# Kernel optimization log

Hardware: AMD Instinct MI355X
Metric: run time of the kernel (lower is better)

## Reference

```python
import jax, jax.numpy as jnp
import numpy as np

N = 50000
E = 800000
IN_CH = 128
HID = 64
HEADS = 4
EPS = 1e-5
NEG_SLOPE = 0.2


def _gat_conv(x, src, dst, W, a_src, a_dst, b, heads, out_ch, concat):
    n = x.shape[0]
    h = (x @ W).reshape(n, heads, out_ch)                      # [N,H,C]
    alpha_src = jnp.sum(h * a_src, axis=-1)                    # [N,H]
    alpha_dst = jnp.sum(h * a_dst, axis=-1)                    # [N,H]
    e = jax.nn.leaky_relu(alpha_src[src] + alpha_dst[dst], NEG_SLOPE)  # [E',H]
    # segment softmax over incoming edges of each destination node
    m = jax.ops.segment_max(e, dst, num_segments=n)            # [N,H]
    e = jnp.exp(e - m[dst])
    denom = jax.ops.segment_sum(e, dst, num_segments=n)        # [N,H]
    alpha = e / denom[dst]                                     # [E',H]
    msg = h[src] * alpha[:, :, None]                           # [E',H,C]
    out = jax.ops.segment_sum(msg, dst, num_segments=n)        # [N,H,C]
    if concat:
        out = out.reshape(n, heads * out_ch)
    else:
        out = out.mean(axis=1)
    return out + b


def _bn_eval(x, gamma, beta, mean, var):
    return (x - mean) * (gamma / jnp.sqrt(var + EPS)) + beta


def setup_inputs() -> dict:
    key = jax.random.key(0)
    ks = jax.random.split(key, 24)
    s = 0.1
    x = jax.random.normal(ks[0], (N, IN_CH), dtype=jnp.float32)
    edge_index = jax.random.randint(ks[1], (2, E), 0, N, dtype=jnp.int32)
    d0, d1 = IN_CH, HID * HEADS
    inp = {
        'x': x, 'edge_index': edge_index,
        # layer 0: in_ch -> hidden, heads=4, concat
        'W0': jax.random.normal(ks[2], (d0, HEADS * HID), jnp.float32) * s,
        'as0': jax.random.normal(ks[3], (HEADS, HID), jnp.float32) * s,
        'ad0': jax.random.normal(ks[4], (HEADS, HID), jnp.float32) * s,
        'b0': jax.random.normal(ks[5], (HEADS * HID,), jnp.float32) * s,
        # layer 1: hidden*heads -> hidden, heads=4, concat
        'W1': jax.random.normal(ks[6], (d1, HEADS * HID), jnp.float32) * s,
        'as1': jax.random.normal(ks[7], (HEADS, HID), jnp.float32) * s,
        'ad1': jax.random.normal(ks[8], (HEADS, HID), jnp.float32) * s,
        'b1': jax.random.normal(ks[9], (HEADS * HID,), jnp.float32) * s,
        # layer 2: hidden*heads -> 1, heads=1, no concat
        'W2': jax.random.normal(ks[10], (d1, 1), jnp.float32) * s,
        'as2': jax.random.normal(ks[11], (1, 1), jnp.float32) * s,
        'ad2': jax.random.normal(ks[12], (1, 1), jnp.float32) * s,
        'b2': jax.random.normal(ks[13], (1,), jnp.float32) * s,
        # batchnorm (eval) params for the two hidden layers
        'g0': jnp.ones((d1,), jnp.float32),
        'be0': jnp.zeros((d1,), jnp.float32),
        'm0': jax.random.normal(ks[14], (d1,), jnp.float32) * s,
        'v0': jnp.ones((d1,), jnp.float32),
        'g1': jnp.ones((d1,), jnp.float32),
        'be1': jnp.zeros((d1,), jnp.float32),
        'm1': jax.random.normal(ks[15], (d1,), jnp.float32) * s,
        'v1': jnp.ones((d1,), jnp.float32),
    }
    return inp


def reference(x, edge_index, W0, as0, ad0, b0, W1, as1, ad1, b1,
              W2, as2, ad2, b2, g0, be0, m0, v0, g1, be1, m1, v1):
    n = x.shape[0]
    loops = jnp.arange(n, dtype=edge_index.dtype)
    src = jnp.concatenate([edge_index[0], loops])  # add self-loops (PyG default)
    dst = jnp.concatenate([edge_index[1], loops])

    # layer 0 (no residual: shapes differ)
    h = _gat_conv(x, src, dst, W0, as0, ad0, b0, HEADS, HID, True)
    h = jax.nn.elu(_bn_eval(h, g0, be0, m0, v0))

    # layer 1 (residual: shapes match)
    res = h
    h = _gat_conv(h, src, dst, W1, as1, ad1, b1, HEADS, HID, True)
    h = jax.nn.elu(_bn_eval(h, g1, be1, m1, v1)) + res

    # output layer: heads=1, concat=False -> [N,1]
    out = _gat_conv(h, src, dst, W2, as2, ad2, b2, 1, 1, False)
    return out.squeeze(-1)
```

## Files before the change

kernel.cpp:

```cpp
#include <hip/hip_runtime.h>
#include <math.h>

#define NEG_SLOPE 0.2f
#define BN_EPS 1e-5f

typedef __attribute__((ext_vector_type(8))) short bf16x8;
typedef __attribute__((ext_vector_type(4))) float f32x4;

static __device__ __forceinline__ unsigned short f2bf(float f){
    unsigned u = __float_as_uint(f);
    u += 0x7FFFu + ((u >> 16) & 1u);
    return (unsigned short)(u >> 16);
}
static __device__ __forceinline__ float bf2f(unsigned short v){
    return __uint_as_float((unsigned)v << 16);
}

static __device__ __forceinline__ void gload_lds16(const void* g, void* l){
    __builtin_amdgcn_global_load_lds(
        (const __attribute__((address_space(1))) void*)g,
        (__attribute__((address_space(3))) void*)l, 16, 0, 0);
}

static __device__ __forceinline__ void repack_one(const float* __restrict__ W,
    unsigned short* __restrict__ whi, unsigned short* __restrict__ wlo, int o)
{
    const int j = o & 7, ln = (o >> 3) & 63, ct = (o >> 9) & 15, kt = o >> 13;
    const int k = kt * 32 + 8 * (ln >> 4) + j;
    const int col = ct * 16 + (ln & 15);
    const float v = W[k * 256 + col];
    const unsigned short hb = f2bf(v);
    whi[o] = hb; wlo[o] = f2bf(v - bf2f(hb));
}

__global__ void prep_kernel(const float* __restrict__ W0,
    unsigned short* __restrict__ w0hi, unsigned short* __restrict__ w0lo,
    const float* __restrict__ W1,
    unsigned short* __restrict__ w1hi, unsigned short* __restrict__ w1lo,
    int* __restrict__ deg, int N)
{
    const int bid = blockIdx.x, t = threadIdx.x;
    if (bid < 128){
        repack_one(W0, w0hi, w0lo, bid * 256 + t);
    } else if (bid < 384){
        repack_one(W1, w1hi, w1lo, (bid - 128) * 256 + t);
    } else {
        const int i = (bid - 384) * 256 + t;
        if (i < N) deg[i] = 1;
    }
}

__global__ __launch_bounds__(256) void mfma_gemm0(
    const float* __restrict__ x,
    const unsigned short* __restrict__ wbhi, const unsigned short* __restrict__ wblo,
    const float* __restrict__ a_s, const float* __restrict__ a_d,
    unsigned short* __restrict__ hout,
    float* __restrict__ asrc, float* __restrict__ adst, int N)
{
    constexpr int K = 128;
    __shared__ float xaf[4][2][64][4];
    __shared__ unsigned short wb[32][512];
    const int t = threadIdx.x, lane = t & 63, wid = t >> 6;
    const int n0 = blockIdx.x * 64;

    f32x4 acc[4][4];
#pragma unroll
    for (int rt = 0; rt < 4; ++rt)
#pragma unroll
        for (int q = 0; q < 4; ++q) acc[rt][q] = (f32x4){0.f, 0.f, 0.f, 0.f};

    for (int kt = 0; kt < K / 32; ++kt){
        __syncthreads();
#pragma unroll
        for (int ii = 0; ii < 2; ++ii){
            const int i = wid * 2 + ii;
            const int rt = i >> 1, half = i & 1;
            int node = n0 + rt * 16 + (lane & 15);
            if (node > N - 1) node = N - 1;
            const float* src = &x[(size_t)node * K + kt * 32 + 8 * (lane >> 4) + half * 4];
            gload_lds16(src, &xaf[rt][half][0][0]);
        }
#pragma unroll
        for (int ii = 0; ii < 8; ++ii){
            const int i = wid * 8 + ii;
            const int ct = i >> 1, plane = i & 1;
            const unsigned short* base = plane ? wblo : wbhi;
            gload_lds16(base + ((size_t)(kt * 16 + ct) * 64 + lane) * 8, &wb[i][0]);
        }
        __syncthreads();

        bf16x8 ahi[4], alo[4];
#pragma unroll
        for (int rt = 0; rt < 4; ++rt){
            const float4 f0 = *(const float4*)&xaf[rt][0][lane][0];
            const float4 f1 = *(const float4*)&xaf[rt][1][lane][0];
            const float fv[8] = {f0.x, f0.y, f0.z, f0.w, f1.x, f1.y, f1.z, f1.w};
#pragma unroll
            for (int j = 0; j < 8; ++j){
                const unsigned short hb = f2bf(fv[j]);
                ahi[rt][j] = (short)hb;
                alo[rt][j] = (short)f2bf(fv[j] - bf2f(hb));
            }
        }

#pragma unroll
        for (int q = 0; q < 4; ++q){
            const int cti = wid * 4 + q;
            const bf16x8 bhi = *(const bf16x8*)&wb[cti * 2 + 0][lane * 8];
            const bf16x8 blo = *(const bf16x8*)&wb[cti * 2 + 1][lane * 8];
#pragma unroll
            for (int rt = 0; rt < 4; ++rt){
                acc[rt][q] = __builtin_amdgcn_mfma_f32_16x16x32_bf16(ahi[rt], bhi, acc[rt][q], 0, 0, 0);
                acc[rt][q] = __builtin_amdgcn_mfma_f32_16x16x32_bf16(alo[rt], bhi, acc[rt][q], 0, 0, 0);
                acc[rt][q] = __builtin_amdgcn_mfma_f32_16x16x32_bf16(ahi[rt], blo, acc[rt][q], 0, 0, 0);
            }
        }
    }

    const int l15 = lane & 15, lg = lane >> 4;
    float avs[4], avd[4];
#pragma unroll
    for (int q = 0; q < 4; ++q){
        avs[q] = a_s[wid * 64 + q * 16 + l15];
        avd[q] = a_d[wid * 64 + q * 16 + l15];
    }
    float sp[4][4], dp[4][4];
#pragma unroll
    for (int rt = 0; rt < 4; ++rt){
#pragma unroll
        for (int reg = 0; reg < 4; ++reg){
            const int node = n0 + rt * 16 + lg * 4 + reg;
            float s = 0.f, d = 0.f;
            unsigned short hv[4];
#pragma unroll
            for (int q = 0; q < 4; ++q){
                const float v = acc[rt][q][reg];
                s = fmaf(v, avs[q], s); d = fmaf(v, avd[q], d);
                hv[q] = f2bf(v);
            }
            if (node < N){
#pragma unroll
                for (int q = 0; q < 4; ++q)
                    hout[(size_t)node * 256 + (wid * 4 + q) * 16 + l15] = hv[q];
            }
            sp[rt][reg] = s; dp[rt][reg] = d;
        }
    }
#pragma unroll
    for (int off = 1; off <= 8; off <<= 1){
#pragma unroll
        for (int rt = 0; rt < 4; ++rt)
#pragma unroll
            for (int reg = 0; reg < 4; ++reg){
                sp[rt][reg] += __shfl_xor(sp[rt][reg], off, 64);
                dp[rt][reg] += __shfl_xor(dp[rt][reg], off, 64);
            }
    }
    if (l15 == 0){
#pragma unroll
        for (int rt = 0; rt < 4; ++rt)
#pragma unroll
            for (int reg = 0; reg < 4; ++reg){
                const int node = n0 + rt * 16 + lg * 4 + reg;
                if (node < N){
                    asrc[(size_t)node * 4 + wid] = sp[rt][reg];
                    adst[(size_t)node * 4 + wid] = dp[rt][reg];
                }
            }
    }
}

__global__ __launch_bounds__(256) void mfma_gemm1(
    const unsigned short* __restrict__ xb,
    const unsigned short* __restrict__ wbhi, const unsigned short* __restrict__ wblo,
    const float* __restrict__ a_s, const float* __restrict__ a_d,
    unsigned short* __restrict__ hout,
    float* __restrict__ asrc, float* __restrict__ adst, int N)
{
    constexpr int K = 256;
    __shared__ unsigned short xab[4][512];
    __shared__ unsigned short wb[32][512];
    const int t = threadIdx.x, lane = t & 63, wid = t >> 6;
    const int n0 = blockIdx.x * 64;

    f32x4 acc[4][4];
#pragma unroll
    for (int rt = 0; rt < 4; ++rt)
#pragma unroll
        for (int q = 0; q < 4; ++q) acc[rt][q] = (f32x4){0.f, 0.f, 0.f, 0.f};

    for (int kt = 0; kt < K / 32; ++kt){
        __syncthreads();
        {
            const int rt = wid;
            int node = n0 + rt * 16 + (lane & 15);
            if (node > N - 1) node = N - 1;
            const unsigned short* src = &xb[(size_t)node * K + kt * 32 + 8 * (lane >> 4)];
            gload_lds16(src, &xab[rt][0]);
        }
#pragma unroll
        for (int ii = 0; ii < 8; ++ii){
            const int i = wid * 8 + ii;
            const int ct = i >> 1, plane = i & 1;
            const unsigned short* base = plane ? wblo : wbhi;
            gload_lds16(base + ((size_t)(kt * 16 + ct) * 64 + lane) * 8, &wb[i][0]);
        }
        __syncthreads();

        bf16x8 a[4];
#pragma unroll
        for (int rt = 0; rt < 4; ++rt)
            a[rt] = *(const bf16x8*)&xab[rt][lane * 8];

#pragma unroll
        for (int q = 0; q < 4; ++q){
            const int cti = wid * 4 + q;
            const bf16x8 bhi = *(const bf16x8*)&wb[cti * 2 + 0][lane * 8];
            const bf16x8 blo = *(const bf16x8*)&wb[cti * 2 + 1][lane * 8];
#pragma unroll
            for (int rt = 0; rt < 4; ++rt){
                acc[rt][q] = __builtin_amdgcn_mfma_f32_16x16x32_bf16(a[rt], bhi, acc[rt][q], 0, 0, 0);
                acc[rt][q] = __builtin_amdgcn_mfma_f32_16x16x32_bf16(a[rt], blo, acc[rt][q], 0, 0, 0);
            }
        }
    }

    const int l15 = lane & 15, lg = lane >> 4;
    float avs[4], avd[4];
#pragma unroll
    for (int q = 0; q < 4; ++q){
        avs[q] = a_s[wid * 64 + q * 16 + l15];
        avd[q] = a_d[wid * 64 + q * 16 + l15];
    }
    float sp[4][4], dp[4][4];
#pragma unroll
    for (int rt = 0; rt < 4; ++rt){
#pragma unroll
        for (int reg = 0; reg < 4; ++reg){
            const int node = n0 + rt * 16 + lg * 4 + reg;
            float s = 0.f, d = 0.f;
            unsigned short hv[4];
#pragma unroll
            for (int q = 0; q < 4; ++q){
                const float v = acc[rt][q][reg];
                s = fmaf(v, avs[q], s); d = fmaf(v, avd[q], d);
                hv[q] = f2bf(v);
            }
            if (node < N){
#pragma unroll
                for (int q = 0; q < 4; ++q)
                    hout[(size_t)node * 256 + (wid * 4 + q) * 16 + l15] = hv[q];
            }
            sp[rt][reg] = s; dp[rt][reg] = d;
        }
    }
#pragma unroll
    for (int off = 1; off <= 8; off <<= 1){
#pragma unroll
        for (int rt = 0; rt < 4; ++rt)
#pragma unroll
            for (int reg = 0; reg < 4; ++reg){
                sp[rt][reg] += __shfl_xor(sp[rt][reg], off, 64);
                dp[rt][reg] += __shfl_xor(dp[rt][reg], off, 64);
            }
    }
    if (l15 == 0){
#pragma unroll
        for (int rt = 0; rt < 4; ++rt)
#pragma unroll
            for (int reg = 0; reg < 4; ++reg){
                const int node = n0 + rt * 16 + lg * 4 + reg;
                if (node < N){
                    asrc[(size_t)node * 4 + wid] = sp[rt][reg];
                    adst[(size_t)node * 4 + wid] = dp[rt][reg];
                }
            }
    }
}

__global__ void deg_hist_kernel(const int* __restrict__ ei, int E, int* __restrict__ deg){
    int e = blockIdx.x * blockDim.x + threadIdx.x;
    if (e < E) atomicAdd(&deg[ei[E + e]], 1);
}

__global__ __launch_bounds__(256) void part_sum_kernel(const int* __restrict__ deg,
                                                       int* __restrict__ bsum, int N)
{
    __shared__ int red[256];
    const int t = threadIdx.x;
    const int i0 = blockIdx.x * 1024 + t * 4;
    int s = 0;
    if (i0 + 3 < N){
        const int4 v = *(const int4*)&deg[i0];
        s = v.x + v.y + v.z + v.w;
    } else {
#pragma unroll
        for (int j = 0; j < 4; ++j) if (i0 + j < N) s += deg[i0 + j];
    }
    red[t] = s; __syncthreads();
    for (int off = 128; off >= 1; off >>= 1){
        if (t < off) red[t] += red[t + off];
        __syncthreads();
    }
    if (t == 0) bsum[blockIdx.x] = red[0];
}

__global__ __launch_bounds__(256) void scan_part_kernel(int* __restrict__ bsum, int nb,
                                                        int* __restrict__ row, int N)
{
    __shared__ int sh[256];
    const int t = threadIdx.x;
    const int v = (t < nb) ? bsum[t] : 0;
    sh[t] = v; __syncthreads();
    for (int off = 1; off < 256; off <<= 1){
        int u = (t >= off) ? sh[t - off] : 0;
        __syncthreads();
        sh[t] += u;
        __syncthreads();
    }
    if (t < nb) bsum[t] = sh[t] - v;
    if (t == nb - 1) row[N] = sh[t];
}

__global__ __launch_bounds__(256) void distribute_kernel(const int* __restrict__ deg,
    const int* __restrict__ bsum, int* __restrict__ row, int* __restrict__ cursor, int N)
{
    __shared__ int ts[256];
    const int t = threadIdx.x;
    const int i0 = blockIdx.x * 1024 + t * 4;
    int d[4]; int s = 0;
#pragma unroll
    for (int j = 0; j < 4; ++j){ d[j] = (i0 + j < N) ? deg[i0 + j] : 0; s += d[j]; }
    ts[t] = s; __syncthreads();
    for (int off = 1; off < 256; off <<= 1){
        int u = (t >= off) ? ts[t - off] : 0;
        __syncthreads();
        ts[t] += u;
        __syncthreads();
    }
    int base = bsum[blockIdx.x] + ts[t] - s;
#pragma unroll
    for (int j = 0; j < 4; ++j){
        if (i0 + j < N){ row[i0 + j] = base; cursor[i0 + j] = base; base += d[j]; }
    }
}

__global__ void scatter_kernel(const int* __restrict__ ei, int E, int N,
                               int* __restrict__ cursor, int* __restrict__ csr)
{
    int e = blockIdx.x * blockDim.x + threadIdx.x;
    if (e >= E + N) return;
    int s, d;
    if (e < E){ s = ei[e]; d = ei[E + e]; } else { s = d = e - E; }
    int pos = atomicAdd(&cursor[d], 1);
    csr[pos] = s;
}

#define DEG_CAP 128
template<bool LAST>
__global__ __launch_bounds__(256) void agg4_kernel(
    const int* __restrict__ row, const int* __restrict__ csr,
    const float* __restrict__ asrc, const float* __restrict__ adst,
    const unsigned short* __restrict__ h,
    const float* __restrict__ b, const float* __restrict__ g,
    const float* __restrict__ be, const float* __restrict__ mean,
    const float* __restrict__ var,
    const unsigned short* __restrict__ res,
    unsigned short* __restrict__ outbf,
    float* __restrict__ outh2,
    const float* __restrict__ W2,
    int N)
{
    __shared__ float plds[4][DEG_CAP * 4];
    __shared__ int   slds[4][DEG_CAP];
    const int wid = threadIdx.x >> 6, lane = threadIdx.x & 63;
    const int node = blockIdx.x * 4 + wid;
    if (node >= N) return;
    const int beg = row[node], end = row[node + 1], deg = end - beg;
    const int degc = deg < DEG_CAP ? deg : DEG_CAP;
    const int head = lane >> 4;

    const float4 ad = *(const float4*)&adst[(size_t)node * 4];

    float d0 = 0.f, d1 = 0.f, d2 = 0.f, d3 = 0.f;
    for (int i = lane; i < deg; i += 64){
        const int s = csr[beg + i];
        const float4 as = *(const float4*)&asrc[(size_t)s * 4];
        float v0 = as.x + ad.x, v1 = as.y + ad.y, v2 = as.z + ad.z, v3 = as.w + ad.w;
        v0 = v0 > 0.f ? v0 : NEG_SLOPE * v0;
        v1 = v1 > 0.f ? v1 : NEG_SLOPE * v1;
        v2 = v2 > 0.f ? v2 : NEG_SLOPE * v2;
        v3 = v3 > 0.f ? v3 : NEG_SLOPE * v3;
        const float p0 = __expf(v0), p1 = __expf(v1);
        const float p2 = __expf(v2), p3 = __expf(v3);
        d0 += p0; d1 += p1; d2 += p2; d3 += p3;
        if (i < DEG_CAP){
            *(float4*)&plds[wid][i * 4] = make_float4(p0, p1, p2, p3);
            slds[wid][i] = s << 9;
        }
    }
    for (int off = 32; off >= 1; off >>= 1){
        d0 += __shfl_xor(d0, off, 64); d1 += __shfl_xor(d1, off, 64);
        d2 += __shfl_xor(d2, off, 64); d3 += __shfl_xor(d3, off, 64);
    }

    float a0 = 0.f, a1 = 0.f, a2 = 0.f, a3 = 0.f;
    {
        const char* hb = (const char*)h + lane * 8;
        const float* pb = &plds[wid][0];
        const int* sb = &slds[wid][0];
        int i = 0;
        for (; i + 8 <= degc; i += 8){
            ushort4 hv[8];
#pragma unroll
            for (int u = 0; u < 8; ++u) hv[u] = *(const ushort4*)(hb + sb[i + u]);
#pragma unroll
            for (int u = 0; u < 8; ++u){
                const float p_ = pb[(i + u) * 4 + head];
                a0 = fmaf(p_, bf2f(hv[u].x), a0); a1 = fmaf(p_, bf2f(hv[u].y), a1);
                a2 = fmaf(p_, bf2f(hv[u].z), a2); a3 = fmaf(p_, bf2f(hv[u].w), a3);
            }
        }
        for (; i < degc; ++i){
            const float p_ = pb[i * 4 + head];
            const ushort4 hv_ = *(const ushort4*)(hb + sb[i]);
            a0 = fmaf(p_, bf2f(hv_.x), a0); a1 = fmaf(p_, bf2f(hv_.y), a1);
            a2 = fmaf(p_, bf2f(hv_.z), a2); a3 = fmaf(p_, bf2f(hv_.w), a3);
        }
    }

    for (int jj = beg + DEG_CAP; jj < end; ++jj){
        const int s = csr[jj];
        const float4 as = *(const float4*)&asrc[(size_t)s * 4];
        float e0 = as.x + ad.x, e1 = as.y + ad.y, e2 = as.z + ad.z, e3 = as.w + ad.w;
        float eh = (head == 0) ? e0 : (head == 1) ? e1 : (head == 2) ? e2 : e3;
        eh = eh > 0.f ? eh : NEG_SLOPE * eh;
        const float p = __expf(eh);
        const ushort4 hv = *(const ushort4*)&h[(size_t)s * 256 + lane * 4];
        a0 = fmaf(p, bf2f(hv.x), a0); a1 = fmaf(p, bf2f(hv.y), a1);
        a2 = fmaf(p, bf2f(hv.z), a2); a3 = fmaf(p, bf2f(hv.w), a3);
    }

    const int l15 = lane & 15;
    const float dsel = (head == 0) ? d0 : (head == 1) ? d1 : (head == 2) ? d2 : d3;
    const float rdi = 1.f / dsel;
    const int c0 = head * 64 + 4 * l15;
    const float4 bv  = *(const float4*)&b[c0];
    const float4 gv  = *(const float4*)&g[c0];
    const float4 bev = *(const float4*)&be[c0];
    const float4 mv  = *(const float4*)&mean[c0];
    const float4 vv4 = *(const float4*)&var[c0];
    const float ava[4]  = {a0, a1, a2, a3};
    const float bva[4]  = {bv.x, bv.y, bv.z, bv.w};
    const float gva[4]  = {gv.x, gv.y, gv.z, gv.w};
    const float beva[4] = {bev.x, bev.y, bev.z, bev.w};
    const float mva[4]  = {mv.x, mv.y, mv.z, mv.w};
    const float vva[4]  = {vv4.x, vv4.y, vv4.z, vv4.w};
    float rh[4] = {0.f, 0.f, 0.f, 0.f};
    if (LAST){
        const ushort4 rv = *(const ushort4*)&res[(size_t)node * 256 + c0];
        rh[0] = bf2f(rv.x); rh[1] = bf2f(rv.y); rh[2] = bf2f(rv.z); rh[3] = bf2f(rv.w);
    }
    float vvv[4];
#pragma unroll
    for (int j = 0; j < 4; ++j){
        float v = ava[j] * rdi + bva[j];
        v = (v - mva[j]) * (gva[j] * rsqrtf(vva[j] + BN_EPS)) + beva[j];
        v = v > 0.f ? v : (__expf(v) - 1.f);
        vvv[j] = v + rh[j];
    }
    if (!LAST){
        ushort4 o4;
        o4.x = f2bf(vvv[0]); o4.y = f2bf(vvv[1]);
        o4.z = f2bf(vvv[2]); o4.w = f2bf(vvv[3]);
        *(ushort4*)&outbf[(size_t)node * 256 + c0] = o4;
    } else {
        const float4 w2v = *(const float4*)&W2[c0];
        float part = vvv[0] * w2v.x + vvv[1] * w2v.y + vvv[2] * w2v.z + vvv[3] * w2v.w;
        for (int off = 32; off >= 1; off >>= 1) part += __shfl_xor(part, off, 64);
        if (lane == 0) outh2[node] = part;
    }
}

__global__ void agg2_kernel(const int* __restrict__ row, const int* __restrict__ csr,
                            const float* __restrict__ h2,
                            const float* __restrict__ as2, const float* __restrict__ ad2,
                            const float* __restrict__ b2, float* __restrict__ out, int N)
{
    const int n = blockIdx.x * blockDim.x + threadIdx.x;
    if (n >= N) return;
    const float A_s = as2[0];
    const float hd  = h2[n] * ad2[0];
    const int beg = row[n], end = row[n + 1];
    float den = 0.f, acc = 0.f;
    for (int i = beg; i < end; ++i){
        const float hv = h2[csr[i]];
        float a = fmaf(A_s, hv, hd);
        a = a > 0.f ? a : NEG_SLOPE * a;
        const float p = __expf(a);
        den += p; acc = fmaf(p, hv, acc);
    }
    out[n] = acc / den + b2[0];
}

extern "C" void kernel_launch(void* const* d_in, const int* in_sizes, int n_in,
                              void* d_out, int out_size, void* d_ws, size_t ws_size,
                              hipStream_t stream)
{
    const float* x   = (const float*)d_in[0];
    const int*   ei  = (const int*)  d_in[1];
    const float* W0  = (const float*)d_in[2];
    const float* as0 = (const float*)d_in[3];
    const float* ad0 = (const float*)d_in[4];
    const float* b0  = (const float*)d_in[5];
    const float* W1  = (const float*)d_in[6];
    const float* as1 = (const float*)d_in[7];
    const float* ad1 = (const float*)d_in[8];
    const float* b1  = (const float*)d_in[9];
    const float* W2  = (const float*)d_in[10];
    const float* as2 = (const float*)d_in[11];
    const float* ad2 = (const float*)d_in[12];
    const float* b2  = (const float*)d_in[13];
    const float* g0  = (const float*)d_in[14];
    const float* be0 = (const float*)d_in[15];
    const float* m0  = (const float*)d_in[16];
    const float* v0  = (const float*)d_in[17];
    const float* g1  = (const float*)d_in[18];
    const float* be1 = (const float*)d_in[19];
    const float* m1  = (const float*)d_in[20];
    const float* v1  = (const float*)d_in[21];

    const int N = in_sizes[0] / 128;
    const int E = in_sizes[1] / 2;
    const int EN = E + N;

    char* w = (char*)d_ws;
    unsigned short* H    = (unsigned short*)w;  w += (size_t)N * 256 * 2;
    unsigned short* P0   = (unsigned short*)w;  w += (size_t)N * 256 * 2;
    float*    asrc   = (float*)w;   w += (size_t)N * 4 * 4;
    float*    adst   = (float*)w;   w += (size_t)N * 4 * 4;
    int*      deg    = (int*)w;     w += (size_t)N * 4;
    int*      cursor = (int*)w;     w += (size_t)N * 4;
    int*      csr    = (int*)w;     w += (size_t)EN * 4;
    float*    h2     = (float*)w;   w += (size_t)N * 4;
    int*      bsum   = (int*)w;     w += 1024;
    unsigned short* Wb0hi = (unsigned short*)w; w += (size_t)128 * 256 * 2;
    unsigned short* Wb0lo = (unsigned short*)w; w += (size_t)128 * 256 * 2;
    unsigned short* Wb1hi = (unsigned short*)w; w += (size_t)256 * 256 * 2;
    unsigned short* Wb1lo = (unsigned short*)w; w += (size_t)256 * 256 * 2;
    int*      rowp   = (int*)w;     w += (size_t)(N + 1) * 4;

    const int gN64  = (N + 63) / 64;
    const int gN4   = (N + 3) / 4;
    const int gNt   = (N + 255) / 256;
    const int gE    = (E + 255) / 256;
    const int gEN   = (EN + 255) / 256;
    const int nb    = (N + 1023) / 1024;

    prep_kernel<<<384 + gNt, 256, 0, stream>>>(W0, Wb0hi, Wb0lo, W1, Wb1hi, Wb1lo, deg, N);
    deg_hist_kernel<<<gE, 256, 0, stream>>>(ei, E, deg);
    part_sum_kernel<<<nb, 256, 0, stream>>>(deg, bsum, N);
    scan_part_kernel<<<1, 256, 0, stream>>>(bsum, nb, rowp, N);
    distribute_kernel<<<nb, 256, 0, stream>>>(deg, bsum, rowp, cursor, N);
    scatter_kernel<<<gEN, 256, 0, stream>>>(ei, E, N, cursor, csr);

    mfma_gemm0<<<gN64, 256, 0, stream>>>(x, Wb0hi, Wb0lo,
                                         as0, ad0, H, asrc, adst, N);
    agg4_kernel<false><<<gN4, 256, 0, stream>>>(rowp, csr, asrc, adst, H,
                                                b0, g0, be0, m0, v0,
                                                nullptr, P0, nullptr, nullptr, N);

    mfma_gemm1<<<gN64, 256, 0, stream>>>(P0, Wb1hi, Wb1lo,
                                         as1, ad1, H, asrc, adst, N);
    agg4_kernel<true><<<gN4, 256, 0, stream>>>(rowp, csr, asrc, adst, H,
                                               b1, g1, be1, m1, v1,
                                               P0, nullptr, h2, W2, N);

    agg2_kernel<<<gNt, 256, 0, stream>>>(rowp, csr, h2, as2, ad2, b2, (float*)d_out, N);
}
```

Measured before the change: 321.1 us.

## Load GEMM operands directly from global into registers, drop LDS staging

Both GEMM kernels stop staging x and the packed weight planes through shared memory with global_load_lds and two barriers per k-step. Each wave now loads its A fragments and B fragments straight into registers from global memory, with the k-loop partially unrolled. The aggregation gather loop is also reduced from an 8-way batched load unroll to a 2-way unroll. This removes LDS traffic and synchronisation, but it gives up sharing the weight tiles across waves, so each wave reads them redundantly from cache. The smaller gather unroll reduces memory-level parallelism.

After: 324.7 us. No clear change (+1.1%).

```diff
diff --git a/kernel.cpp b/kernel.cpp
--- a/kernel.cpp
+++ b/kernel.cpp
@@ -14,12 +14,6 @@
 }
 static __device__ __forceinline__ float bf2f(unsigned short v){
     return __uint_as_float((unsigned)v << 16);
-}
-
-static __device__ __forceinline__ void gload_lds16(const void* g, void* l){
-    __builtin_amdgcn_global_load_lds(
-        (const __attribute__((address_space(1))) void*)g,
-        (__attribute__((address_space(3))) void*)l, 16, 0, 0);
 }
 
 static __device__ __forceinline__ void repack_one(const float* __restrict__ W,
@@ -58,10 +52,19 @@
     float* __restrict__ asrc, float* __restrict__ adst, int N)
 {
     constexpr int K = 128;
-    __shared__ float xaf[4][2][64][4];
-    __shared__ unsigned short wb[32][512];
     const int t = threadIdx.x, lane = t & 63, wid = t >> 6;
     const int n0 = blockIdx.x * 64;
+    const int l15 = lane & 15, lg = lane >> 4;
+
+    const float* ap[4];
+#pragma unroll
+    for (int rt = 0; rt < 4; ++rt){
+        int node = n0 + rt * 16 + l15;
+        if (node > N - 1) node = N - 1;
+        ap[rt] = &x[(size_t)node * K + 8 * lg];
+    }
+    const unsigned short* bph = &wbhi[((size_t)(wid * 4) * 64 + lane) * 8];
+    const unsigned short* bpl = &wblo[((size_t)(wid * 4) * 64 + lane) * 8];
 
     f32x4 acc[4][4];
 #pragma unroll
@@ -69,32 +72,25 @@
 #pragma unroll
         for (int q = 0; q < 4; ++q) acc[rt][q] = (f32x4){0.f, 0.f, 0.f, 0.f};
 
+#pragma unroll 2
     for (int kt = 0; kt < K / 32; ++kt){
-        __syncthreads();
-#pragma unroll
-        for (int ii = 0; ii < 2; ++ii){
-            const int i = wid * 2 + ii;
-            const int rt = i >> 1, half = i & 1;
-            int node = n0 + rt * 16 + (lane & 15);
-            if (node > N - 1) node = N - 1;
-            const float* src = &x[(size_t)node * K + kt * 32 + 8 * (lane >> 4) + half * 4];
-            gload_lds16(src, &xaf[rt][half][0][0]);
-        }
-#pragma unroll
-        for (int ii = 0; ii < 8; ++ii){
-            const int i = wid * 8 + ii;
-            const int ct = i >> 1, plane = i & 1;
-            const unsigned short* base = plane ? wblo : wbhi;
-            gload_lds16(base + ((size_t)(kt * 16 + ct) * 64 + lane) * 8, &wb[i][0]);
-        }
-        __syncthreads();
-
+        bf16x8 bhi[4], blo[4];
+#pragma unroll
+        for (int q = 0; q < 4; ++q){
+            bhi[q] = *(const bf16x8*)(bph + ((size_t)kt * 16 + q) * 512);
+            blo[q] = *(const bf16x8*)(bpl + ((size_t)kt * 16 + q) * 512);
+        }
+        float4 f0[4], f1[4];
+#pragma unroll
+        for (int rt = 0; rt < 4; ++rt){
+            f0[rt] = *(const float4*)(ap[rt] + kt * 32);
+            f1[rt] = *(const float4*)(ap[rt] + kt * 32 + 4);
+        }
         bf16x8 ahi[4], alo[4];
 #pragma unroll
         for (int rt = 0; rt < 4; ++rt){
-            const float4 f0 = *(const float4*)&xaf[rt][0][lane][0];
-            const float4 f1 = *(const float4*)&xaf[rt][1][lane][0];
-            const float fv[8] = {f0.x, f0.y, f0.z, f0.w, f1.x, f1.y, f1.z, f1.w};
+            const float fv[8] = {f0[rt].x, f0[rt].y, f0[rt].z, f0[rt].w,
+                                 f1[rt].x, f1[rt].y, f1[rt].z, f1[rt].w};
 #pragma unroll
             for (int j = 0; j < 8; ++j){
                 const unsigned short hb = f2bf(fv[j]);
@@ -102,22 +98,16 @@
                 alo[rt][j] = (short)f2bf(fv[j] - bf2f(hb));
             }
         }
-
-#pragma unroll
-        for (int q = 0; q < 4; ++q){
-            const int cti = wid * 4 + q;
-            const bf16x8 bhi = *(const bf16x8*)&wb[cti * 2 + 0][lane * 8];
-            const bf16x8 blo = *(const bf16x8*)&wb[cti * 2 + 1][lane * 8];
+#pragma unroll
+        for (int q = 0; q < 4; ++q)
 #pragma unroll
             for (int rt = 0; rt < 4; ++rt){
-                acc[rt][q] = __builtin_amdgcn_mfma_f32_16x16x32_bf16(ahi[rt], bhi, acc[rt][q], 0, 0, 0);
-                acc[rt][q] = __builtin_amdgcn_mfma_f32_16x16x32_bf16(alo[rt], bhi, acc[rt][q], 0, 0, 0);
-                acc[rt][q] = __builtin_amdgcn_mfma_f32_16x16x32_bf16(ahi[rt], blo, acc[rt][q], 0, 0, 0);
-            }
-        }
-    }
-
-    const int l15 = lane & 15, lg = lane >> 4;
+                acc[rt][q] = __builtin_amdgcn_mfma_f32_16x16x32_bf16(ahi[rt], bhi[q], acc[rt][q], 0, 0, 0);
+                acc[rt][q] = __builtin_amdgcn_mfma_f32_16x16x32_bf16(alo[rt], bhi[q], acc[rt][q], 0, 0, 0);
+                acc[rt][q] = __builtin_amdgcn_mfma_f32_16x16x32_bf16(ahi[rt], blo[q], acc[rt][q], 0, 0, 0);
+            }
+    }
+
     float avs[4], avd[4];
 #pragma unroll
     for (int q = 0; q < 4; ++q){
@@ -178,10 +168,19 @@
     float* __restrict__ asrc, float* __restrict__ adst, int N)
 {
     constexpr int K = 256;
-    __shared__ unsigned short xab[4][512];
-    __shared__ unsigned short wb[32][512];
     const int t = threadIdx.x, lane = t & 63, wid = t >> 6;
     const int n0 = blockIdx.x * 64;
+    const int l15 = lane & 15, lg = lane >> 4;
+
+    const unsigned short* ap[4];
+#pragma unroll
+    for (int rt = 0; rt < 4; ++rt){
+        int node = n0 + rt * 16 + l15;
+        if (node > N - 1) node = N - 1;
+        ap[rt] = &xb[(size_t)node * K + 8 * lg];
+    }
+    const unsigned short* bph = &wbhi[((size_t)(wid * 4) * 64 + lane) * 8];
+    const unsigned short* bpl = &wblo[((size_t)(wid * 4) * 64 + lane) * 8];
 
     f32x4 acc[4][4];
 #pragma unroll
@@ -189,43 +188,28 @@
 #pragma unroll
         for (int q = 0; q < 4; ++q) acc[rt][q] = (f32x4){0.f, 0.f, 0.f, 0.f};
 
+#pragma unroll 2
     for (int kt = 0; kt < K / 32; ++kt){
-        __syncthreads();
-        {
-            const int rt = wid;
-            int node = n0 + rt * 16 + (lane & 15);
-            if (node > N - 1) node = N - 1;
-            const unsigned short* src = &xb[(size_t)node * K + kt * 32 + 8 * (lane >> 4)];
-            gload_lds16(src, &xab[rt][0]);
-        }
-#pragma unroll
-        for (int ii = 0; ii < 8; ++ii){
-            const int i = wid * 8 + ii;
-            const int ct = i >> 1, plane = i & 1;
-            const unsigned short* base = plane ? wblo : wbhi;
-            gload_lds16(base + ((size_t)(kt * 16 + ct) * 64 + lane) * 8, &wb[i][0]);
-        }
-        __syncthreads();
-
+        bf16x8 bhi[4], blo[4];
+#pragma unroll
+        for (int q = 0; q < 4; ++q){
+            bhi[q] = *(const bf16x8*)(bph + ((size_t)kt * 16 + q) * 512);
+            blo[q] = *(const bf16x8*)(bpl + ((size_t)kt * 16 + q) * 512);
+        }
         bf16x8 a[4];
 #pragma unroll
         for (int rt = 0; rt < 4; ++rt)
-            a[rt] = *(const bf16x8*)&xab[rt][lane * 8];
-
-#pragma unroll
-        for (int q = 0; q < 4; ++q){
-            const int cti = wid * 4 + q;
-            const bf16x8 bhi = *(const bf16x8*)&wb[cti * 2 + 0][lane * 8];
-            const bf16x8 blo = *(const bf16x8*)&wb[cti * 2 + 1][lane * 8];
+            a[rt] = *(const bf16x8*)(ap[rt] + kt * 32);
+
+#pragma unroll
+        for (int q = 0; q < 4; ++q)
 #pragma unroll
             for (int rt = 0; rt < 4; ++rt){
-                acc[rt][q] = __builtin_amdgcn_mfma_f32_16x16x32_bf16(a[rt], bhi, acc[rt][q], 0, 0, 0);
-                acc[rt][q] = __builtin_amdgcn_mfma_f32_16x16x32_bf16(a[rt], blo, acc[rt][q], 0, 0, 0);
-            }
-        }
-    }
-
-    const int l15 = lane & 15, lg = lane >> 4;
+                acc[rt][q] = __builtin_amdgcn_mfma_f32_16x16x32_bf16(a[rt], bhi[q], acc[rt][q], 0, 0, 0);
+                acc[rt][q] = __builtin_amdgcn_mfma_f32_16x16x32_bf16(a[rt], blo[q], acc[rt][q], 0, 0, 0);
+            }
+    }
+
     float avs[4], avd[4];
 #pragma unroll
     for (int q = 0; q < 4; ++q){
@@ -409,24 +393,20 @@
         const char* hb = (const char*)h + lane * 8;
         const float* pb = &plds[wid][0];
         const int* sb = &slds[wid][0];
+#define EDGE_BODY(slot)                                                        \
+        {                                                                      \
+            const float p_ = pb[(slot) * 4 + head];                            \
+            const ushort4 hv_ = *(const ushort4*)(hb + sb[slot]);              \
+            a0 = fmaf(p_, bf2f(hv_.x), a0); a1 = fmaf(p_, bf2f(hv_.y), a1);    \
+            a2 = fmaf(p_, bf2f(hv_.z), a2); a3 = fmaf(p_, bf2f(hv_.w), a3);    \
+        }
         int i = 0;
-        for (; i + 8 <= degc; i += 8){
-            ushort4 hv[8];
-#pragma unroll
-            for (int u = 0; u < 8; ++u) hv[u] = *(const ushort4*)(hb + sb[i + u]);
-#pragma unroll
-            for (int u = 0; u < 8; ++u){
-                const float p_ = pb[(i + u) * 4 + head];
-                a0 = fmaf(p_, bf2f(hv[u].x), a0); a1 = fmaf(p_, bf2f(hv[u].y), a1);
-                a2 = fmaf(p_, bf2f(hv[u].z), a2); a3 = fmaf(p_, bf2f(hv[u].w), a3);
-            }
-        }
-        for (; i < degc; ++i){
-            const float p_ = pb[i * 4 + head];
-            const ushort4 hv_ = *(const ushort4*)(hb + sb[i]);
-            a0 = fmaf(p_, bf2f(hv_.x), a0); a1 = fmaf(p_, bf2f(hv_.y), a1);
-            a2 = fmaf(p_, bf2f(hv_.z), a2); a3 = fmaf(p_, bf2f(hv_.w), a3);
-        }
+        for (; i + 2 <= degc; i += 2){
+            EDGE_BODY(i);
+            EDGE_BODY(i + 1);
+        }
+        for (; i < degc; ++i) EDGE_BODY(i);
+#undef EDGE_BODY
     }
 
     for (int jj = beg + DEG_CAP; jj < end; ++jj){
```
